# Performance work log

Measured on AMD Instinct MI355X. Metric: run time of the kernel, lower is better.

The kernel has to match this reference:

```python
import jax, jax.numpy as jnp
import numpy as np

N_EMBD = 1024
N_HEAD = 16
B, T = 1, 4096
EPS = 1e-5


def layer_norm(x, w):
    mu = jnp.mean(x, axis=-1, keepdims=True)
    var = jnp.var(x, axis=-1, keepdims=True)
    return (x - mu) / jnp.sqrt(var + EPS) * w


def setup_inputs() -> dict:
    key = jax.random.key(0)
    ks = jax.random.split(key, 6)
    s = 0.02
    return {
        "x": jax.random.normal(ks[0], (B, T, N_EMBD), dtype=jnp.float32),
        "w_qkv": jax.random.normal(ks[1], (N_EMBD, 3 * N_EMBD), dtype=jnp.float32) * s,
        "w_attn_proj": jax.random.normal(ks[2], (N_EMBD, N_EMBD), dtype=jnp.float32) * s,
        "w_fc": jax.random.normal(ks[3], (N_EMBD, 4 * N_EMBD), dtype=jnp.float32) * s,
        "w_mlp_proj": jax.random.normal(ks[4], (4 * N_EMBD, N_EMBD), dtype=jnp.float32) * s,
        "ln1_w": jnp.ones((N_EMBD,), dtype=jnp.float32),
        "ln2_w": jnp.ones((N_EMBD,), dtype=jnp.float32),
    }


def reference(x, w_qkv, w_attn_proj, w_fc, w_mlp_proj, ln1_w, ln2_w):
    Bq, Tq, C = x.shape
    hs = C // N_HEAD

    # --- attention branch (pre-norm) ---
    h = layer_norm(x, ln1_w)
    qkv = h @ w_qkv  # [B,T,3C]
    q, k, v = jnp.split(qkv, 3, axis=-1)
    q = q.reshape(Bq, Tq, N_HEAD, hs).transpose(0, 2, 1, 3)  # [B,H,T,hs]
    k = k.reshape(Bq, Tq, N_HEAD, hs).transpose(0, 2, 1, 3)
    v = v.reshape(Bq, Tq, N_HEAD, hs).transpose(0, 2, 1, 3)

    scores = jnp.einsum("bhqd,bhkd->bhqk", q, k) * (1.0 / jnp.sqrt(jnp.float32(hs)))
    causal = jnp.tril(jnp.ones((Tq, Tq), dtype=bool))
    scores = jnp.where(causal, scores, -jnp.inf)
    weights = jax.nn.softmax(scores, axis=-1)  # dropout=0 -> identity
    out = jnp.einsum("bhqk,bhkd->bhqd", weights, v)
    out = out.transpose(0, 2, 1, 3).reshape(Bq, Tq, C)
    x = x + out @ w_attn_proj

    # --- MLP branch (pre-norm) ---
    h = layer_norm(x, ln2_w)
    h = jax.nn.gelu(h @ w_fc, approximate=False)  # nn.GELU default is exact
    x = x + h @ w_mlp_proj
    return x
```

## Files before the change

### kernel.cpp

```cpp
#include <hip/hip_runtime.h>
#include <cstdint>

typedef __attribute__((ext_vector_type(8))) short short8;
typedef __attribute__((ext_vector_type(4))) float f32x4;

__device__ __forceinline__ float b2f(unsigned short u) {
    return __uint_as_float(((unsigned int)u) << 16);
}
__device__ __forceinline__ unsigned short f2b(float f) {
    unsigned int u = __float_as_uint(f);
    u += 0x7FFFu + ((u >> 16) & 1u);
    return (unsigned short)(u >> 16);
}

__device__ __forceinline__ void gload_lds16(const unsigned short* g, unsigned short* l) {
    __builtin_amdgcn_global_load_lds(
        (const __attribute__((address_space(1))) uint32_t*)g,
        (__attribute__((address_space(3))) uint32_t*)l, 16, 0, 0);
}

__global__ __launch_bounds__(256) void k_transpose_bf16(
        const float* __restrict__ w, unsigned short* __restrict__ wT, int K, int N) {
    __shared__ float tile[32][33];
    int n0 = blockIdx.x * 32, k0 = blockIdx.y * 32;
    int tx = threadIdx.x, ty = threadIdx.y;
#pragma unroll
    for (int i = 0; i < 4; i++)
        tile[ty + 8 * i][tx] = w[(size_t)(k0 + ty + 8 * i) * N + n0 + tx];
    __syncthreads();
#pragma unroll
    for (int i = 0; i < 4; i++)
        wT[(size_t)(n0 + ty + 8 * i) * K + k0 + tx] = f2b(tile[tx][ty + 8 * i]);
}

__global__ __launch_bounds__(256) void k_layernorm(
        const float* __restrict__ x, const float* __restrict__ w,
        unsigned short* __restrict__ out) {
    int row = blockIdx.x, tid = threadIdx.x;
    const float4* xr = (const float4*)(x + (size_t)row * 1024);
    float4 v = xr[tid];
    float s  = v.x + v.y + v.z + v.w;
    float ss = v.x * v.x + v.y * v.y + v.z * v.z + v.w * v.w;
#pragma unroll
    for (int off = 32; off >= 1; off >>= 1) {
        s  += __shfl_down(s, off);
        ss += __shfl_down(ss, off);
    }
    __shared__ float red[10];
    if ((tid & 63) == 0) { red[tid >> 6] = s; red[4 + (tid >> 6)] = ss; }
    __syncthreads();
    if (tid == 0) {
        float S  = red[0] + red[1] + red[2] + red[3];
        float SS = red[4] + red[5] + red[6] + red[7];
        float mu  = S * (1.0f / 1024.0f);
        float var = SS * (1.0f / 1024.0f) - mu * mu;
        red[8] = mu; red[9] = rsqrtf(var + 1e-5f);
    }
    __syncthreads();
    float mu = red[8], rs = red[9];
    float4 wv = ((const float4*)w)[tid];
    ushort4 pk;
    pk.x = f2b((v.x - mu) * rs * wv.x);
    pk.y = f2b((v.y - mu) * rs * wv.y);
    pk.z = f2b((v.z - mu) * rs * wv.z);
    pk.w = f2b((v.w - mu) * rs * wv.w);
    *(ushort4*)(out + (size_t)row * 1024 + tid * 4) = pk;
}

template <int EPI, int TN>
__global__ __launch_bounds__(256) void k_gemm_bt(
        const unsigned short* __restrict__ A, const unsigned short* __restrict__ BT,
        const float* __restrict__ RES, void* __restrict__ OUT,
        int M, int N, int K) {
    constexpr int MI = (TN == 128) ? 4 : 2;
    __shared__ __align__(16) unsigned short As[128 * 64];
    __shared__ __align__(16) unsigned short Bs[TN * 64];
    int tid  = threadIdx.x;
    int lane = tid & 63, wave = tid >> 6;
    int quad = lane >> 4, qr = lane & 15;
    int wm_off = (TN == 128) ? (wave >> 1) * 64 : wave * 32;
    int wn_off = (TN == 128) ? (wave & 1) * 64 : 0;
    int m0 = blockIdx.y * 128, n0 = blockIdx.x * TN;
    int lrow = lane >> 3;
    int gcol = 8 * (((lane & 7) - lrow) & 7);
    int cswz[2];
#pragma unroll
    for (int kk = 0; kk < 2; kk++) cswz[kk] = 8 * (((kk * 4) + quad + (qr & 7)) & 7);
    f32x4 acc[MI][4] = {};
    for (int k0 = 0; k0 < K; k0 += 64) {
        __syncthreads();
#pragma unroll
        for (int t = 0; t < 4; t++) {
            int rowb = wave * 32 + t * 8;
            gload_lds16(&A[(size_t)(m0 + rowb + lrow) * K + k0 + gcol], &As[rowb * 64]);
        }
#pragma unroll
        for (int t = 0; t < TN / 32; t++) {
            int rowb = wave * (TN / 4) + t * 8;
            gload_lds16(&BT[(size_t)(n0 + rowb + lrow) * K + k0 + gcol], &Bs[rowb * 64]);
        }
        __syncthreads();
#pragma unroll
        for (int kk = 0; kk < 2; kk++) {
            short8 af[MI], bfr[4];
#pragma unroll
            for (int i = 0; i < MI; i++) af[i]  = *(const short8*)&As[(wm_off + i * 16 + qr) * 64 + cswz[kk]];
#pragma unroll
            for (int j = 0; j < 4; j++)  bfr[j] = *(const short8*)&Bs[(wn_off + j * 16 + qr) * 64 + cswz[kk]];
#pragma unroll
            for (int i = 0; i < MI; i++)
#pragma unroll
                for (int j = 0; j < 4; j++)
                    acc[i][j] = __builtin_amdgcn_mfma_f32_16x16x32_bf16(af[i], bfr[j], acc[i][j], 0, 0, 0);
        }
    }
#pragma unroll
    for (int i = 0; i < MI; i++) {
#pragma unroll
        for (int j = 0; j < 4; j++) {
#pragma unroll
            for (int r = 0; r < 4; r++) {
                int row = m0 + wm_off + i * 16 + quad * 4 + r;
                int col = n0 + wn_off + j * 16 + qr;
                size_t idx = (size_t)row * N + col;
                float v = acc[i][j][r];
                if (EPI == 1)      ((unsigned short*)OUT)[idx] = f2b(v);
                else if (EPI == 2) ((float*)OUT)[idx] = RES[idx] + v;
                else {
                    float u = v * fmaf(v * v, 0.035677408f, 0.79788456f);
                    float e = fminf(u * 2.885390082f, 80.0f);
                    float t = exp2f(e);
                    float g = v * t / (t + 1.0f);
                    ((unsigned short*)OUT)[idx] = f2b(g);
                }
            }
        }
    }
}

__global__ __launch_bounds__(256) void k_attn(
        const unsigned short* __restrict__ qkv, unsigned short* __restrict__ out) {
    __shared__ unsigned short Ks[128][72];
    __shared__ unsigned short Vt[64][136];
    __shared__ unsigned short Ps[4][16][136];

    const float C1 = 0.18033688f;
    const float C2 = 5.77078016f;

    int l = blockIdx.x;
    int h = l & 15;
    int qb = 63 - (l >> 4);
    int q0 = qb * 64;

    int tid = threadIdx.x;
    int wave = tid >> 6, lane = tid & 63;
    int lane16 = lane & 15, quad = lane >> 4;

    {
        int srow = tid >> 2, sc0 = (tid & 3) * 16;
        size_t base = (size_t)(q0 + srow) * 3072 + h * 64 + sc0;
        *(uint4*)&Ks[srow][sc0]     = *(const uint4*)&qkv[base];
        *(uint4*)&Ks[srow][sc0 + 8] = *(const uint4*)&qkv[base + 8];
    }
    __syncthreads();
    short8 aq0 = *(const short8*)&Ks[wave * 16 + lane16][quad * 8];
    short8 aq1 = *(const short8*)&Ks[wave * 16 + lane16][32 + quad * 8];

    f32x4 Oacc[4] = {};
    float l_part[4] = {0.f, 0.f, 0.f, 0.f};

    int srow = tid >> 1, sc0 = (tid & 1) * 32;
    int vk = (lane & 31) * 2;
    int d0 = wave * 16 + (lane >> 5) * 8;

    uint4 pk0, pk1, pk2, pk3, pv0, pv1, pv2, pv3;
    {
        size_t base = (size_t)srow * 3072 + 1024 + h * 64 + sc0;
        pk0 = *(const uint4*)&qkv[base];
        pk1 = *(const uint4*)&qkv[base + 8];
        pk2 = *(const uint4*)&qkv[base + 16];
        pk3 = *(const uint4*)&qkv[base + 24];
        size_t vb0 = (size_t)vk * 3072 + 2048 + h * 64 + d0;
        pv0 = *(const uint4*)&qkv[vb0];
        pv1 = *(const uint4*)&qkv[vb0 + 3072];
        size_t vb1 = (size_t)(64 + vk) * 3072 + 2048 + h * 64 + d0;
        pv2 = *(const uint4*)&qkv[vb1];
        pv3 = *(const uint4*)&qkv[vb1 + 3072];
    }

    for (int kc = 0; kc <= qb; kc += 2) {
        __syncthreads();
        {
            *(uint4*)&Ks[srow][sc0]      = pk0;
            *(uint4*)&Ks[srow][sc0 + 8]  = pk1;
            *(uint4*)&Ks[srow][sc0 + 16] = pk2;
            *(uint4*)&Ks[srow][sc0 + 24] = pk3;
        }
        {
            const unsigned short* pe0 = (const unsigned short*)&pv0;
            const unsigned short* po0 = (const unsigned short*)&pv1;
            const unsigned short* pe1 = (const unsigned short*)&pv2;
            const unsigned short* po1 = (const unsigned short*)&pv3;
#pragma unroll
            for (int j = 0; j < 8; j++) {
                *(uint32_t*)&Vt[d0 + j][vk]      = (uint32_t)pe0[j] | ((uint32_t)po0[j] << 16);
                *(uint32_t*)&Vt[d0 + j][64 + vk] = (uint32_t)pe1[j] | ((uint32_t)po1[j] << 16);
            }
        }
        __syncthreads();

        if (kc + 2 <= qb) {
            size_t base = (size_t)((kc + 2) * 64 + srow) * 3072 + 1024 + h * 64 + sc0;
            pk0 = *(const uint4*)&qkv[base];
            pk1 = *(const uint4*)&qkv[base + 8];
            pk2 = *(const uint4*)&qkv[base + 16];
            pk3 = *(const uint4*)&qkv[base + 24];
            size_t vb0 = (size_t)((kc + 2) * 64 + vk) * 3072 + 2048 + h * 64 + d0;
            pv0 = *(const uint4*)&qkv[vb0];
            pv1 = *(const uint4*)&qkv[vb0 + 3072];
            size_t vb1 = (size_t)((kc + 3) * 64 + vk) * 3072 + 2048 + h * 64 + d0;
            pv2 = *(const uint4*)&qkv[vb1];
            pv3 = *(const uint4*)&qkv[vb1 + 3072];
        }

        f32x4 sacc[8] = {};
#pragma unroll
        for (int kt = 0; kt < 8; kt++) {
            short8 bk0 = *(const short8*)&Ks[kt * 16 + lane16][quad * 8];
            short8 bk1 = *(const short8*)&Ks[kt * 16 + lane16][32 + quad * 8];
            sacc[kt] = __builtin_amdgcn_mfma_f32_16x16x32_bf16(aq0, bk0, sacc[kt], 0, 0, 0);
            sacc[kt] = __builtin_amdgcn_mfma_f32_16x16x32_bf16(aq1, bk1, sacc[kt], 0, 0, 0);
        }

        bool domask = (kc + 2 > qb);
#pragma unroll
        for (int r = 0; r < 4; r++) {
            int qrow = q0 + wave * 16 + quad * 4 + r;
#pragma unroll
            for (int kt = 0; kt < 8; kt++) {
                float s = sacc[kt][r];
                if (domask) {
                    int key = kc * 64 + kt * 16 + lane16;
                    s = (key <= qrow) ? s : -__builtin_inff();
                }
                float p = exp2f(fmaf(s, C1, -C2));
                l_part[r] += p;
                Ps[wave][quad * 4 + r][kt * 16 + lane16] = f2b(p);
            }
        }

#pragma unroll
        for (int s = 0; s < 4; s++) {
            short8 ap = *(const short8*)&Ps[wave][lane16][s * 32 + quad * 8];
#pragma unroll
            for (int dt = 0; dt < 4; dt++) {
                short8 bv = *(const short8*)&Vt[dt * 16 + lane16][s * 32 + quad * 8];
                Oacc[dt] = __builtin_amdgcn_mfma_f32_16x16x32_bf16(ap, bv, Oacc[dt], 0, 0, 0);
            }
        }
    }

    float invl[4];
#pragma unroll
    for (int r = 0; r < 4; r++) {
        float lf = l_part[r];
        lf += __shfl_xor(lf, 1);
        lf += __shfl_xor(lf, 2);
        lf += __shfl_xor(lf, 4);
        lf += __shfl_xor(lf, 8);
        invl[r] = 1.0f / lf;
    }
#pragma unroll
    for (int dt = 0; dt < 4; dt++) {
#pragma unroll
        for (int r = 0; r < 4; r++) {
            int qrow = q0 + wave * 16 + quad * 4 + r;
            out[(size_t)qrow * 1024 + h * 64 + dt * 16 + lane16] = f2b(Oacc[dt][r] * invl[r]);
        }
    }
}

extern "C" void kernel_launch(void* const* d_in, const int* in_sizes, int n_in,
                              void* d_out, int out_size, void* d_ws, size_t ws_size,
                              hipStream_t stream) {
    const float* x      = (const float*)d_in[0];
    const float* w_qkv  = (const float*)d_in[1];
    const float* w_attn = (const float*)d_in[2];
    const float* w_fc   = (const float*)d_in[3];
    const float* w_mlp  = (const float*)d_in[4];
    const float* ln1w   = (const float*)d_in[5];
    const float* ln2w   = (const float*)d_in[6];

    char* ws = (char*)d_ws;
    unsigned short* h      = (unsigned short*)(ws + 0);
    unsigned short* wqkvT  = (unsigned short*)(ws + 8388608);
    unsigned short* wattnT = (unsigned short*)(ws + 14680064);
    unsigned short* wfcT   = (unsigned short*)(ws + 16777216);
    unsigned short* wmlpT  = (unsigned short*)(ws + 25165824);
    unsigned short* qkv    = (unsigned short*)(ws + 33554432);
    unsigned short* attno  = (unsigned short*)(ws + 58720256);
    float*          x2     = (float*)(ws + 67108864);
    unsigned short* fcact  = (unsigned short*)(ws + 83886080);
    float* outF = (float*)d_out;

    dim3 tb(32, 8);
    k_transpose_bf16<<<dim3(96, 32),  tb, 0, stream>>>(w_qkv,  wqkvT,  1024, 3072);
    k_transpose_bf16<<<dim3(32, 32),  tb, 0, stream>>>(w_attn, wattnT, 1024, 1024);
    k_transpose_bf16<<<dim3(128, 32), tb, 0, stream>>>(w_fc,   wfcT,   1024, 4096);
    k_transpose_bf16<<<dim3(32, 128), tb, 0, stream>>>(w_mlp,  wmlpT,  4096, 1024);

    k_layernorm<<<4096, 256, 0, stream>>>(x, ln1w, h);
    k_gemm_bt<1, 128><<<dim3(24, 32), 256, 0, stream>>>(h, wqkvT, nullptr, qkv, 4096, 3072, 1024);
    k_attn<<<1024, 256, 0, stream>>>(qkv, attno);
    k_gemm_bt<2, 64><<<dim3(16, 32), 256, 0, stream>>>(attno, wattnT, x, x2, 4096, 1024, 1024);
    k_layernorm<<<4096, 256, 0, stream>>>(x2, ln2w, h);
    k_gemm_bt<3, 128><<<dim3(32, 32), 256, 0, stream>>>(h, wfcT, nullptr, fcact, 4096, 4096, 1024);
    k_gemm_bt<2, 64><<<dim3(16, 32), 256, 0, stream>>>(fcact, wmlpT, x2, outF, 4096, 1024, 4096);
}
```

Measured before the change: 373.2 us.

## Prefetch GEMM tiles into registers to overlap global loads with MFMA

The GEMM main loop no longer uses direct global-to-LDS loads. Each tile is now loaded into registers one iteration ahead, then written to swizzled LDS after the barrier. The next tile's global reads are issued before the MFMA compute, so memory latency overlaps with math without adding a second LDS buffer. The cost is extra VGPRs and an explicit register-to-LDS store pass, which could lower occupancy.

```diff
diff --git a/kernel.cpp b/kernel.cpp
--- a/kernel.cpp
+++ b/kernel.cpp
@@ -11,12 +11,6 @@
     unsigned int u = __float_as_uint(f);
     u += 0x7FFFu + ((u >> 16) & 1u);
     return (unsigned short)(u >> 16);
-}
-
-__device__ __forceinline__ void gload_lds16(const unsigned short* g, unsigned short* l) {
-    __builtin_amdgcn_global_load_lds(
-        (const __attribute__((address_space(1))) uint32_t*)g,
-        (__attribute__((address_space(3))) uint32_t*)l, 16, 0, 0);
 }
 
 __global__ __launch_bounds__(256) void k_transpose_bf16(
@@ -73,6 +67,7 @@
         const float* __restrict__ RES, void* __restrict__ OUT,
         int M, int N, int K) {
     constexpr int MI = (TN == 128) ? 4 : 2;
+    constexpr int NB = TN / 32;
     __shared__ __align__(16) unsigned short As[128 * 64];
     __shared__ __align__(16) unsigned short Bs[TN * 64];
     int tid  = threadIdx.x;
@@ -81,25 +76,44 @@
     int wm_off = (TN == 128) ? (wave >> 1) * 64 : wave * 32;
     int wn_off = (TN == 128) ? (wave & 1) * 64 : 0;
     int m0 = blockIdx.y * 128, n0 = blockIdx.x * TN;
-    int lrow = lane >> 3;
-    int gcol = 8 * (((lane & 7) - lrow) & 7);
+    int arow[4], acol[4];
+#pragma unroll
+    for (int t = 0; t < 4; t++) {
+        int id = t * 256 + tid;
+        arow[t] = id >> 3;
+        acol[t] = (id & 7) * 8;
+    }
     int cswz[2];
 #pragma unroll
     for (int kk = 0; kk < 2; kk++) cswz[kk] = 8 * (((kk * 4) + quad + (qr & 7)) & 7);
+
+    uint4 pa[4], pb[NB];
+    {
+#pragma unroll
+        for (int t = 0; t < 4; t++)
+            pa[t] = *(const uint4*)&A[(size_t)(m0 + arow[t]) * K + acol[t]];
+#pragma unroll
+        for (int t = 0; t < NB; t++)
+            pb[t] = *(const uint4*)&BT[(size_t)(n0 + arow[t]) * K + acol[t]];
+    }
     f32x4 acc[MI][4] = {};
     for (int k0 = 0; k0 < K; k0 += 64) {
         __syncthreads();
 #pragma unroll
-        for (int t = 0; t < 4; t++) {
-            int rowb = wave * 32 + t * 8;
-            gload_lds16(&A[(size_t)(m0 + rowb + lrow) * K + k0 + gcol], &As[rowb * 64]);
-        }
-#pragma unroll
-        for (int t = 0; t < TN / 32; t++) {
-            int rowb = wave * (TN / 4) + t * 8;
-            gload_lds16(&BT[(size_t)(n0 + rowb + lrow) * K + k0 + gcol], &Bs[rowb * 64]);
-        }
+        for (int t = 0; t < 4; t++)
+            *(uint4*)&As[arow[t] * 64 + ((acol[t] + 8 * (arow[t] & 7)) & 63)] = pa[t];
+#pragma unroll
+        for (int t = 0; t < NB; t++)
+            *(uint4*)&Bs[arow[t] * 64 + ((acol[t] + 8 * (arow[t] & 7)) & 63)] = pb[t];
         __syncthreads();
+        if (k0 + 64 < K) {
+#pragma unroll
+            for (int t = 0; t < 4; t++)
+                pa[t] = *(const uint4*)&A[(size_t)(m0 + arow[t]) * K + k0 + 64 + acol[t]];
+#pragma unroll
+            for (int t = 0; t < NB; t++)
+                pb[t] = *(const uint4*)&BT[(size_t)(n0 + arow[t]) * K + k0 + 64 + acol[t]];
+        }
 #pragma unroll
         for (int kk = 0; kk < 2; kk++) {
             short8 af[MI], bfr[4];
```

New measurement: 750.4 us. 101% more time.

## Register-prefetch GEMM tiles instead of direct global-to-LDS loads

Applied to the files above, without the earlier changes.

Replaces the global_load_lds direct-to-LDS copies in the bf16 GEMM with register prefetching. The next K tile is loaded into registers while MFMAs run on the current LDS tile, then written to LDS with an XOR-style swizzle. It also sets launch_bounds to 2 blocks per CU. The aim is to overlap global memory latency with compute, at the cost of extra VGPRs and explicit LDS store instructions.

```diff
diff --git a/kernel.cpp b/kernel.cpp
--- a/kernel.cpp
+++ b/kernel.cpp
@@ -11,12 +11,6 @@
     unsigned int u = __float_as_uint(f);
     u += 0x7FFFu + ((u >> 16) & 1u);
     return (unsigned short)(u >> 16);
-}
-
-__device__ __forceinline__ void gload_lds16(const unsigned short* g, unsigned short* l) {
-    __builtin_amdgcn_global_load_lds(
-        (const __attribute__((address_space(1))) uint32_t*)g,
-        (__attribute__((address_space(3))) uint32_t*)l, 16, 0, 0);
 }
 
 __global__ __launch_bounds__(256) void k_transpose_bf16(
@@ -68,7 +62,7 @@
 }
 
 template <int EPI, int TN>
-__global__ __launch_bounds__(256) void k_gemm_bt(
+__global__ __launch_bounds__(256, 2) void k_gemm_bt(
         const unsigned short* __restrict__ A, const unsigned short* __restrict__ BT,
         const float* __restrict__ RES, void* __restrict__ OUT,
         int M, int N, int K) {
@@ -81,25 +75,56 @@
     int wm_off = (TN == 128) ? (wave >> 1) * 64 : wave * 32;
     int wn_off = (TN == 128) ? (wave & 1) * 64 : 0;
     int m0 = blockIdx.y * 128, n0 = blockIdx.x * TN;
-    int lrow = lane >> 3;
-    int gcol = 8 * (((lane & 7) - lrow) & 7);
+    int r0 = tid >> 3;
+    int c0 = (tid & 7) * 8;
+    int cs = 8 * (((tid & 7) + (r0 & 7)) & 7);
     int cswz[2];
 #pragma unroll
     for (int kk = 0; kk < 2; kk++) cswz[kk] = 8 * (((kk * 4) + quad + (qr & 7)) & 7);
+
+    const unsigned short* Ap = A  + (size_t)(m0 + r0) * K + c0;
+    const unsigned short* Bp = BT + (size_t)(n0 + r0) * K + c0;
+    const size_t sA = (size_t)32 * K;
+
+    uint4 pa0, pa1, pa2, pa3, pb0, pb1, pb2, pb3;
+    pa0 = *(const uint4*)(Ap);
+    pa1 = *(const uint4*)(Ap + sA);
+    pa2 = *(const uint4*)(Ap + 2 * sA);
+    pa3 = *(const uint4*)(Ap + 3 * sA);
+    pb0 = *(const uint4*)(Bp);
+    pb1 = *(const uint4*)(Bp + sA);
+    if constexpr (TN == 128) {
+        pb2 = *(const uint4*)(Bp + 2 * sA);
+        pb3 = *(const uint4*)(Bp + 3 * sA);
+    }
+
     f32x4 acc[MI][4] = {};
     for (int k0 = 0; k0 < K; k0 += 64) {
         __syncthreads();
-#pragma unroll
-        for (int t = 0; t < 4; t++) {
-            int rowb = wave * 32 + t * 8;
-            gload_lds16(&A[(size_t)(m0 + rowb + lrow) * K + k0 + gcol], &As[rowb * 64]);
-        }
-#pragma unroll
-        for (int t = 0; t < TN / 32; t++) {
-            int rowb = wave * (TN / 4) + t * 8;
-            gload_lds16(&BT[(size_t)(n0 + rowb + lrow) * K + k0 + gcol], &Bs[rowb * 64]);
+        *(uint4*)&As[(r0)      * 64 + cs] = pa0;
+        *(uint4*)&As[(32 + r0) * 64 + cs] = pa1;
+        *(uint4*)&As[(64 + r0) * 64 + cs] = pa2;
+        *(uint4*)&As[(96 + r0) * 64 + cs] = pa3;
+        *(uint4*)&Bs[(r0)      * 64 + cs] = pb0;
+        *(uint4*)&Bs[(32 + r0) * 64 + cs] = pb1;
+        if constexpr (TN == 128) {
+            *(uint4*)&Bs[(64 + r0) * 64 + cs] = pb2;
+            *(uint4*)&Bs[(96 + r0) * 64 + cs] = pb3;
         }
         __syncthreads();
+        if (k0 + 64 < K) {
+            int k = k0 + 64;
+            pa0 = *(const uint4*)(Ap + k);
+            pa1 = *(const uint4*)(Ap + sA + k);
+            pa2 = *(const uint4*)(Ap + 2 * sA + k);
+            pa3 = *(const uint4*)(Ap + 3 * sA + k);
+            pb0 = *(const uint4*)(Bp + k);
+            pb1 = *(const uint4*)(Bp + sA + k);
+            if constexpr (TN == 128) {
+                pb2 = *(const uint4*)(Bp + 2 * sA + k);
+                pb3 = *(const uint4*)(Bp + 3 * sA + k);
+            }
+        }
 #pragma unroll
         for (int kk = 0; kk < 2; kk++) {
             short8 af[MI], bfr[4];
```

Measured after the change: 371.6 us. No clear change (-0.5%).
